# Kernel tuning notes

Hardware: AMD Instinct MI355X
Metric: run time of the kernel (lower is better)

The kernel has to match this reference:

```python
import jax, jax.numpy as jnp
import numpy as np

EMBED_SIZE = 1024
HEADS = 16
HEAD_DIM = EMBED_SIZE // HEADS


def setup_inputs() -> dict:
    key = jax.random.key(0)
    k1, k2, k3, k4 = jax.random.split(key, 4)
    N, L = 4, 2048
    return {
        "values": jax.random.normal(k1, (N, L, EMBED_SIZE), dtype=jnp.float32),
        "keys": jax.random.normal(k2, (N, L, EMBED_SIZE), dtype=jnp.float32),
        "query": jax.random.normal(k3, (N, L, EMBED_SIZE), dtype=jnp.float32),
        "w_out": jax.random.normal(k4, (EMBED_SIZE, EMBED_SIZE), dtype=jnp.float32) * (1.0 / np.sqrt(EMBED_SIZE)),
        "b_out": jnp.zeros((EMBED_SIZE,), dtype=jnp.float32),
    }


def reference(values, keys, query, w_out, b_out):
    N, q_len, _ = query.shape
    v_len = values.shape[1]
    k_len = keys.shape[1]
    # split heads: (N, L, H, D). NOTE: source never applies the per-head
    # q/k/v Linear layers in forward, so raw inputs are used directly.
    v = values.reshape(N, v_len, HEADS, HEAD_DIM)
    k = keys.reshape(N, k_len, HEADS, HEAD_DIM)
    q = query.reshape(N, q_len, HEADS, HEAD_DIM)
    # energy: (N, H, Q, K); scale by sqrt(embed_size) as in the source
    energy = jnp.einsum('nqhd,nkhd->nhqk', q, k)
    attn = jax.nn.softmax(energy / jnp.sqrt(jnp.float32(EMBED_SIZE)), axis=3)
    out = jnp.einsum('nhql,nlhd->nqhd', attn, v).reshape(N, q_len, EMBED_SIZE)
    # fc_out: x @ W.T + b (torch Linear convention)
    return out @ w_out.T + b_out
```

## Files before the change

### kernel.cpp

```cpp
#include <hip/hip_runtime.h>
#include <hip/hip_bf16.h>

#define NB 4
#define LSEQ 2048
#define NH 16
#define HD 64
#define EMB 1024

typedef __attribute__((ext_vector_type(8))) short bf16x8;
typedef __attribute__((ext_vector_type(4))) float f32x4;
typedef __attribute__((ext_vector_type(16))) float f32x16;
typedef __attribute__((ext_vector_type(2))) unsigned int uint2v;

__device__ __forceinline__ unsigned short f2bf(float x) {
    union { float f; unsigned u; } v; v.f = x;
    unsigned r = v.u + 0x7fff + ((v.u >> 16) & 1);
    return (unsigned short)(r >> 16);
}

__device__ __forceinline__ float exp2_fast(float x) {
#if __has_builtin(__builtin_amdgcn_exp2f)
    return __builtin_amdgcn_exp2f(x);
#else
    float r; asm("v_exp_f32 %0, %1\n\ts_nop 1" : "=v"(r) : "v"(x)); return r;
#endif
}

__device__ __forceinline__ unsigned pack_bf2(float lo, float hi) {
    union { __hip_bfloat162 h2; unsigned u; } cv;
    cv.h2 = __float22bfloat162_rn(make_float2(lo, hi));
    return cv.u;
}

__device__ __forceinline__ void plswap(unsigned &a, unsigned &b) {
#if __has_builtin(__builtin_amdgcn_permlane32_swap)
    uint2v r = __builtin_amdgcn_permlane32_swap(a, b, false, false);
    a = r[0]; b = r[1];
#else
    asm volatile("s_nop 0\n\tv_permlane32_swap_b32 %0, %1\n\ts_nop 0"
                 : "+v"(a), "+v"(b));
#endif
}

__device__ __forceinline__ void async16(void* lds, const void* g) {
    __builtin_amdgcn_global_load_lds(
        (const __attribute__((address_space(1))) unsigned int*)g,
        (__attribute__((address_space(3))) unsigned int*)lds, 16, 0, 0);
}

__global__ void wconv_kernel(const float* __restrict__ Wf, unsigned short* __restrict__ Wb) {
    int i = (blockIdx.x * 256 + threadIdx.x) * 4;
    float4 v = *(const float4*)(Wf + i);
    ushort4 o = { f2bf(v.x), f2bf(v.y), f2bf(v.z), f2bf(v.w) };
    *(ushort4*)(Wb + i) = o;
}

__global__ void k_prep(const float* __restrict__ Kf, unsigned short* __restrict__ Kb) {
    int idx = blockIdx.x * 256 + threadIdx.x;
    int c   = idx & 7;
    int key = (idx >> 3) & 2047;
    int h   = (idx >> 14) & 15;
    int n   = idx >> 18;
    const float* src = Kf + (size_t)(n * LSEQ + key) * EMB + h * HD + c * 8;
    float4 a = *(const float4*)src;
    float4 b = *(const float4*)(src + 4);
    unsigned short* dst = Kb + (((size_t)(n * NH + h) * LSEQ + key) << 6)
                             + ((c ^ (key & 7)) << 3);
    ushort4 o0 = { f2bf(a.x), f2bf(a.y), f2bf(a.z), f2bf(a.w) };
    ushort4 o1 = { f2bf(b.x), f2bf(b.y), f2bf(b.z), f2bf(b.w) };
    *(ushort4*)dst = o0;
    *(ushort4*)(dst + 4) = o1;
}

__global__ void v_prep(const float* __restrict__ Vf, unsigned short* __restrict__ Vt) {
    int b = blockIdx.x;
    int kt = b & 31, h = (b >> 5) & 15, n = b >> 9;
    const float* src = Vf + (size_t)(n * LSEQ + kt * 64) * EMB + h * HD;
    unsigned short* dst = Vt + ((size_t)b << 12);
    for (int t = threadIdx.x; t < 512; t += 256) {
        int d = t >> 3, c = t & 7;
        const float* s = src + (size_t)(c * 8) * EMB + d;
        ushort4 o0, o1;
        o0.x = f2bf(s[0 * EMB]); o0.y = f2bf(s[1 * EMB]);
        o0.z = f2bf(s[2 * EMB]); o0.w = f2bf(s[3 * EMB]);
        o1.x = f2bf(s[4 * EMB]); o1.y = f2bf(s[5 * EMB]);
        o1.z = f2bf(s[6 * EMB]); o1.w = f2bf(s[7 * EMB]);
        unsigned short* p = dst + (d << 6) + ((c ^ (d & 7)) << 3);
        *(ushort4*)p = o0;
        *(ushort4*)(p + 4) = o1;
    }
}

__global__ __launch_bounds__(256, 2)
void attn8_kernel(const float* __restrict__ Qq, const unsigned short* __restrict__ Kb,
                  const unsigned short* __restrict__ Vt, unsigned short* __restrict__ X)
{
    __shared__ unsigned short Kl[2][4096];
    __shared__ unsigned short Vl[2][4096];

    const int tid  = threadIdx.x;
    const int lane = tid & 63;
    const int w    = tid >> 6;
    const int l31  = lane & 31;
    const int hl   = lane >> 5;
    const int swz7 = lane & 7;
    const int l    = ((blockIdx.x & 7) << 6) + (blockIdx.x >> 3);
    const int nh   = l >> 3;
    const int qtile = l & 7;
    const int n = nh >> 4, h = nh & 15;
    const int qrow0 = qtile * 256 + w * 64;

    const float qscale = 0.03125f * 1.44269504f;
    bf16x8 qf[2][4];
    #pragma unroll
    for (int g = 0; g < 2; ++g) {
        const float* qp = Qq + (size_t)(n * LSEQ + qrow0 + g * 32 + l31) * EMB + h * HD + hl * 8;
        #pragma unroll
        for (int dk = 0; dk < 4; ++dk) {
            bf16x8 t;
            #pragma unroll
            for (int e = 0; e < 8; ++e) t[e] = (short)f2bf(qp[dk * 16 + e] * qscale);
            qf[g][dk] = t;
        }
    }

    f32x16 oaccT[2][2];
    #pragma unroll
    for (int g = 0; g < 2; ++g)
        #pragma unroll
        for (int db = 0; db < 2; ++db)
            #pragma unroll
            for (int e = 0; e < 16; ++e) oaccT[g][db][e] = 0.f;
    float lp[2] = {0.f, 0.f};

    const unsigned short* kg0 = Kb + ((size_t)nh << 17);
    const unsigned short* vg0 = Vt + ((size_t)nh << 17);
    const int t8 = tid << 3;

    async16(&Kl[0][t8],        kg0 + t8);
    async16(&Kl[0][t8 + 2048], kg0 + t8 + 2048);
    async16(&Vl[0][t8],        vg0 + t8);
    async16(&Vl[0][t8 + 2048], vg0 + t8 + 2048);
    asm volatile("s_waitcnt vmcnt(0)" ::: "memory");
    __syncthreads();

    int cur = 0;
    for (int kt = 0; kt < LSEQ / 64; ++kt) {
        if (kt + 1 < LSEQ / 64) {
            const unsigned short* kg = kg0 + ((kt + 1) << 12) + t8;
            const unsigned short* vg = vg0 + ((kt + 1) << 12) + t8;
            async16(&Kl[cur ^ 1][t8],        kg);
            async16(&Kl[cur ^ 1][t8 + 2048], kg + 2048);
            async16(&Vl[cur ^ 1][t8],        vg);
            async16(&Vl[cur ^ 1][t8 + 2048], vg + 2048);
        }

        #pragma unroll
        for (int kb = 0; kb < 2; ++kb) {
            f32x16 sk[2];
            #pragma unroll
            for (int g = 0; g < 2; ++g)
                #pragma unroll
                for (int e = 0; e < 16; ++e) sk[g][e] = 0.f;
            #pragma unroll
            for (int dk = 0; dk < 4; ++dk) {
                bf16x8 ka = *(const bf16x8*)&Kl[cur][((kb * 32 + l31) << 6) + (((2 * dk + hl) ^ swz7) << 3)];
                #pragma unroll
                for (int g = 0; g < 2; ++g)
                    sk[g] = __builtin_amdgcn_mfma_f32_32x32x16_bf16(ka, qf[g][dk], sk[g], 0, 0, 0);
            }

            unsigned wgt[2][4][2];
            #pragma unroll
            for (int g = 0; g < 2; ++g) {
                float p[16];
                #pragma unroll
                for (int e = 0; e < 16; ++e) p[e] = exp2_fast(sk[g][e]);
                {
                    float t0 = (p[0] + p[1]) + (p[2] + p[3]);
                    float t1 = (p[4] + p[5]) + (p[6] + p[7]);
                    float t2 = (p[8] + p[9]) + (p[10] + p[11]);
                    float t3 = (p[12] + p[13]) + (p[14] + p[15]);
                    lp[g] += (t0 + t1) + (t2 + t3);
                }
                #pragma unroll
                for (int gg = 0; gg < 4; ++gg) {
                    wgt[g][gg][0] = pack_bf2(p[4 * gg + 0], p[4 * gg + 1]);
                    wgt[g][gg][1] = pack_bf2(p[4 * gg + 2], p[4 * gg + 3]);
                }
                plswap(wgt[g][0][0], wgt[g][1][0]); plswap(wgt[g][0][1], wgt[g][1][1]);
                plswap(wgt[g][2][0], wgt[g][3][0]); plswap(wgt[g][2][1], wgt[g][3][1]);
            }

            #pragma unroll
            for (int ks = 0; ks < 2; ++ks) {
                #pragma unroll
                for (int db = 0; db < 2; ++db) {
                    bf16x8 va = *(const bf16x8*)&Vl[cur][((db * 32 + l31) << 6) + (((4 * kb + 2 * ks + hl) ^ swz7) << 3)];
                    #pragma unroll
                    for (int g = 0; g < 2; ++g) {
                        union { unsigned u[4]; bf16x8 v; } pu;
                        pu.u[0] = wgt[g][2 * ks + 0][0];
                        pu.u[1] = wgt[g][2 * ks + 0][1];
                        pu.u[2] = wgt[g][2 * ks + 1][0];
                        pu.u[3] = wgt[g][2 * ks + 1][1];
                        oaccT[g][db] = __builtin_amdgcn_mfma_f32_32x32x16_bf16(va, pu.v, oaccT[g][db], 0, 0, 0);
                    }
                }
            }
        }

        asm volatile("s_waitcnt vmcnt(0)" ::: "memory");
        __syncthreads();
        cur ^= 1;
    }

    #pragma unroll
    for (int g = 0; g < 2; ++g) {
        const float ltot = lp[g] + __shfl_xor(lp[g], 32);
        const float rcp = 1.0f / ltot;
        unsigned ow0[4][2], ow1[4][2];
        #pragma unroll
        for (int gg = 0; gg < 4; ++gg) {
            ow0[gg][0] = pack_bf2(oaccT[g][0][4 * gg + 0] * rcp, oaccT[g][0][4 * gg + 1] * rcp);
            ow0[gg][1] = pack_bf2(oaccT[g][0][4 * gg + 2] * rcp, oaccT[g][0][4 * gg + 3] * rcp);
            ow1[gg][0] = pack_bf2(oaccT[g][1][4 * gg + 0] * rcp, oaccT[g][1][4 * gg + 1] * rcp);
            ow1[gg][1] = pack_bf2(oaccT[g][1][4 * gg + 2] * rcp, oaccT[g][1][4 * gg + 3] * rcp);
        }
        #pragma unroll
        for (int gg = 0; gg < 4; ++gg) {
            plswap(ow0[gg][0], ow1[gg][0]);
            plswap(ow0[gg][1], ow1[gg][1]);
        }
        unsigned short* xrow = X + (size_t)(n * LSEQ + qrow0 + g * 32 + l31) * EMB + h * HD + hl * 32;
        #pragma unroll
        for (int gg = 0; gg < 4; ++gg) {
            uint4 st = { ow0[gg][0], ow0[gg][1], ow1[gg][0], ow1[gg][1] };
            *(uint4*)(xrow + 8 * gg) = st;
        }
    }
}

#define KPAD 72
#define PPAD 72

__global__ __launch_bounds__(256, 2)
void attn_kernel(const float* __restrict__ Vv, const float* __restrict__ Kk,
                 const float* __restrict__ Qq, unsigned short* __restrict__ X)
{
    __shared__ unsigned short Klds[64 * KPAD];
    __shared__ unsigned short Vtlds[64 * KPAD];
    __shared__ unsigned short Plds[4 * 16 * PPAD];

    const int tid  = threadIdx.x;
    const int lane = tid & 63;
    const int w    = tid >> 6;
    const int l15  = lane & 15;
    const int l4   = lane >> 4;
    const int qtile = blockIdx.x;
    const int nh    = blockIdx.y;
    const int n = nh >> 4, h = nh & 15;

    bf16x8 qf[2];
    {
        const int qrow = qtile * 64 + w * 16 + l15;
        const float* qp = Qq + (size_t)(n * LSEQ + qrow) * EMB + h * HD + l4 * 8;
        for (int kk = 0; kk < 2; ++kk) {
            bf16x8 t;
            #pragma unroll
            for (int e = 0; e < 8; ++e) t[e] = (short)f2bf(qp[kk * 32 + e] * 0.03125f);
            qf[kk] = t;
        }
    }

    f32x4 oacc[4];
    #pragma unroll
    for (int f = 0; f < 4; ++f) oacc[f] = (f32x4){0.f, 0.f, 0.f, 0.f};
    float mrun[4], lrun[4];
    #pragma unroll
    for (int r = 0; r < 4; ++r) { mrun[r] = -1e30f; lrun[r] = 0.f; }

    for (int kt = 0; kt < LSEQ / 64; ++kt) {
        __syncthreads();
        for (int i = tid; i < 1024; i += 256) {
            const int row = i >> 4;
            const int c4  = (i & 15) * 4;
            const size_t gb = (size_t)(n * LSEQ + kt * 64 + row) * EMB + h * HD + c4;
            const float4 kv = *(const float4*)(Kk + gb);
            const float4 vv = *(const float4*)(Vv + gb);
            ushort4 k4 = { f2bf(kv.x), f2bf(kv.y), f2bf(kv.z), f2bf(kv.w) };
            *(ushort4*)&Klds[row * KPAD + c4] = k4;
            Vtlds[(c4 + 0) * KPAD + row] = f2bf(vv.x);
            Vtlds[(c4 + 1) * KPAD + row] = f2bf(vv.y);
            Vtlds[(c4 + 2) * KPAD + row] = f2bf(vv.z);
            Vtlds[(c4 + 3) * KPAD + row] = f2bf(vv.w);
        }
        __syncthreads();

        f32x4 s[4];
        #pragma unroll
        for (int f = 0; f < 4; ++f) {
            f32x4 acc = (f32x4){0.f, 0.f, 0.f, 0.f};
            #pragma unroll
            for (int kk = 0; kk < 2; ++kk) {
                bf16x8 kb = *(const bf16x8*)&Klds[(f * 16 + l15) * KPAD + kk * 32 + l4 * 8];
                acc = __builtin_amdgcn_mfma_f32_16x16x32_bf16(qf[kk], kb, acc, 0, 0, 0);
            }
            s[f] = acc;
        }

        float mnew[4], corr[4];
        #pragma unroll
        for (int r = 0; r < 4; ++r) {
            float m0 = fmaxf(fmaxf(s[0][r], s[1][r]), fmaxf(s[2][r], s[3][r]));
            #pragma unroll
            for (int msk = 1; msk < 16; msk <<= 1) m0 = fmaxf(m0, __shfl_xor(m0, msk));
            mnew[r] = fmaxf(mrun[r], m0);
            corr[r] = __expf(mrun[r] - mnew[r]);
        }
        float psum[4] = {0.f, 0.f, 0.f, 0.f};
        #pragma unroll
        for (int f = 0; f < 4; ++f) {
            #pragma unroll
            for (int r = 0; r < 4; ++r) {
                float p = __expf(s[f][r] - mnew[r]);
                psum[r] += p;
                Plds[(w * 16 + l4 * 4 + r) * PPAD + f * 16 + l15] = f2bf(p);
            }
        }
        #pragma unroll
        for (int r = 0; r < 4; ++r) {
            float t = psum[r];
            #pragma unroll
            for (int msk = 1; msk < 16; msk <<= 1) t += __shfl_xor(t, msk);
            lrun[r] = lrun[r] * corr[r] + t;
            mrun[r] = mnew[r];
        }
        #pragma unroll
        for (int f = 0; f < 4; ++f) {
            #pragma unroll
            for (int r = 0; r < 4; ++r) oacc[f][r] *= corr[r];
        }
        __syncthreads();

        #pragma unroll
        for (int ks = 0; ks < 2; ++ks) {
            bf16x8 pa = *(const bf16x8*)&Plds[(w * 16 + l15) * PPAD + ks * 32 + l4 * 8];
            #pragma unroll
            for (int f = 0; f < 4; ++f) {
                bf16x8 vb = *(const bf16x8*)&Vtlds[(f * 16 + l15) * KPAD + ks * 32 + l4 * 8];
                oacc[f] = __builtin_amdgcn_mfma_f32_16x16x32_bf16(pa, vb, oacc[f], 0, 0, 0);
            }
        }
    }

    #pragma unroll
    for (int f = 0; f < 4; ++f) {
        #pragma unroll
        for (int r = 0; r < 4; ++r) {
            const int qrow = qtile * 64 + w * 16 + l4 * 4 + r;
            const float o = oacc[f][r] / lrun[r];
            X[(size_t)(n * LSEQ + qrow) * EMB + h * HD + f * 16 + l15] = f2bf(o);
        }
    }
}

__global__ __launch_bounds__(256, 2)
void proj3_kernel(const unsigned short* __restrict__ X, const unsigned short* __restrict__ Wb,
                  const float* __restrict__ bias, float* __restrict__ out)
{
    __shared__ unsigned short Al[2][8192];
    __shared__ unsigned short Bl[2][8192];

    const int tid  = threadIdx.x;
    const int lane = tid & 63;
    const int w    = tid >> 6;
    const int l15  = lane & 15;
    const int l4   = lane >> 4;
    const int bm = blockIdx.y;
    const int bn = blockIdx.x;
    const int wr = (w >> 1) * 64;
    const int wc = (w & 1) * 64;

    f32x4 acc[4][4];
    #pragma unroll
    for (int i = 0; i < 4; ++i)
        #pragma unroll
        for (int j = 0; j < 4; ++j) acc[i][j] = (f32x4){0.f, 0.f, 0.f, 0.f};

    int srow[4], soff[4];
    #pragma unroll
    for (int j = 0; j < 4; ++j) {
        const int cid = tid + j * 256;
        srow[j] = cid >> 3;
        const int c = cid & 7;
        soff[j] = ((c ^ (srow[j] & 7)) << 3);
    }

#define PROJ_STAGE(buf, k0)                                                          \
    {                                                                                \
        _Pragma("unroll")                                                            \
        for (int j = 0; j < 4; ++j) {                                                \
            const int cid = tid + j * 256;                                           \
            async16(&Al[buf][cid << 3],                                              \
                    &X [(size_t)(bm * 128 + srow[j]) * EMB + (k0) + soff[j]]);       \
            async16(&Bl[buf][cid << 3],                                              \
                    &Wb[(size_t)(bn * 128 + srow[j]) * EMB + (k0) + soff[j]]);       \
        }                                                                            \
    }

    PROJ_STAGE(0, 0)
    asm volatile("s_waitcnt vmcnt(0)" ::: "memory");
    __syncthreads();

    int cur = 0;
    for (int k0 = 0; k0 < EMB; k0 += 64) {
        if (k0 + 64 < EMB) PROJ_STAGE(cur ^ 1, k0 + 64)

        #pragma unroll
        for (int kk = 0; kk < 2; ++kk) {
            bf16x8 af[4], bfr[4];
            #pragma unroll
            for (int i = 0; i < 4; ++i) {
                const int row = wr + i * 16 + l15;
                af[i] = *(const bf16x8*)&Al[cur][(row << 6) + (((kk * 4 + l4) ^ (row & 7)) << 3)];
            }
            #pragma unroll
            for (int j = 0; j < 4; ++j) {
                const int row = wc + j * 16 + l15;
                bfr[j] = *(const bf16x8*)&Bl[cur][(row << 6) + (((kk * 4 + l4) ^ (row & 7)) << 3)];
            }
            #pragma unroll
            for (int i = 0; i < 4; ++i)
                #pragma unroll
                for (int j = 0; j < 4; ++j)
                    acc[i][j] = __builtin_amdgcn_mfma_f32_16x16x32_bf16(af[i], bfr[j], acc[i][j], 0, 0, 0);
        }

        asm volatile("s_waitcnt vmcnt(0)" ::: "memory");
        __syncthreads();
        cur ^= 1;
    }

    #pragma unroll
    for (int i = 0; i < 4; ++i) {
        const int row = bm * 128 + wr + i * 16 + l4 * 4;
        #pragma unroll
        for (int j = 0; j < 4; ++j) {
            const int col = bn * 128 + wc + j * 16 + l15;
            const float bj = bias[col];
            #pragma unroll
            for (int r = 0; r < 4; ++r)
                out[(size_t)(row + r) * EMB + col] = acc[i][j][r] + bj;
        }
    }
}

extern "C" void kernel_launch(void* const* d_in, const int* in_sizes, int n_in,
                              void* d_out, int out_size, void* d_ws, size_t ws_size,
                              hipStream_t stream) {
    const float* Vv   = (const float*)d_in[0];
    const float* Kk   = (const float*)d_in[1];
    const float* Qq   = (const float*)d_in[2];
    const float* Wf   = (const float*)d_in[3];
    const float* bias = (const float*)d_in[4];
    float* out = (float*)d_out;

    unsigned short* X  = (unsigned short*)d_ws;
    unsigned short* Wb = (unsigned short*)((char*)d_ws + (size_t)16 * 1024 * 1024);
    const size_t need = (size_t)50 * 1024 * 1024;

    wconv_kernel<<<dim3(EMB * EMB / 1024), 256, 0, stream>>>(Wf, Wb);

    if (ws_size >= need) {
        unsigned short* Kb = (unsigned short*)((char*)d_ws + (size_t)18 * 1024 * 1024);
        unsigned short* Vt = (unsigned short*)((char*)d_ws + (size_t)34 * 1024 * 1024);
        k_prep<<<dim3(4096), 256, 0, stream>>>(Kk, Kb);
        v_prep<<<dim3(2048), 256, 0, stream>>>(Vv, Vt);
        attn8_kernel<<<dim3(512), 256, 0, stream>>>(Qq, Kb, Vt, X);
    } else {
        attn_kernel<<<dim3(LSEQ / 64, NB * NH), 256, 0, stream>>>(Vv, Kk, Qq, X);
    }

    proj3_kernel<<<dim3(EMB / 128, NB * LSEQ / 128), 256, 0, stream>>>(X, Wb, bias, out);
}
```

Baseline: 138.9 us.

## Transpose V through LDS, double attention K-tile, add setprio and grouped proj tiling

The V preparation kernel now reads coalesced float4 rows into a padded LDS tile and transposes from there, replacing strided global reads. The attention kernel stages 128 keys per iteration instead of 64, which halves the number of barriers and doubles LDS use per block. s_setprio is raised around MFMA sections in both attention and projection. The projection launch is remapped to a 1D grid with a grouped block order meant to improve L2 reuse. The larger LDS footprint may reduce occupancy.

```diff
diff --git a/kernel.cpp b/kernel.cpp
--- a/kernel.cpp
+++ b/kernel.cpp
@@ -72,19 +72,28 @@
     *(ushort4*)(dst + 4) = o1;
 }
 
-__global__ void v_prep(const float* __restrict__ Vf, unsigned short* __restrict__ Vt) {
-    int b = blockIdx.x;
-    int kt = b & 31, h = (b >> 5) & 15, n = b >> 9;
+__global__ void v_prep2(const float* __restrict__ Vf, unsigned short* __restrict__ Vt) {
+    __shared__ float T[64][65];
+    const int tid = threadIdx.x;
+    const int b = blockIdx.x;
+    const int kt = b & 31, h = (b >> 5) & 15, n = b >> 9;
     const float* src = Vf + (size_t)(n * LSEQ + kt * 64) * EMB + h * HD;
     unsigned short* dst = Vt + ((size_t)b << 12);
-    for (int t = threadIdx.x; t < 512; t += 256) {
-        int d = t >> 3, c = t & 7;
-        const float* s = src + (size_t)(c * 8) * EMB + d;
-        ushort4 o0, o1;
-        o0.x = f2bf(s[0 * EMB]); o0.y = f2bf(s[1 * EMB]);
-        o0.z = f2bf(s[2 * EMB]); o0.w = f2bf(s[3 * EMB]);
-        o1.x = f2bf(s[4 * EMB]); o1.y = f2bf(s[5 * EMB]);
-        o1.z = f2bf(s[6 * EMB]); o1.w = f2bf(s[7 * EMB]);
+
+    for (int i = tid; i < 1024; i += 256) {
+        const int key = i >> 4;
+        const int c4  = (i & 15) * 4;
+        const float4 v = *(const float4*)(src + (size_t)key * EMB + c4);
+        T[key][c4 + 0] = v.x; T[key][c4 + 1] = v.y;
+        T[key][c4 + 2] = v.z; T[key][c4 + 3] = v.w;
+    }
+    __syncthreads();
+    for (int i = tid; i < 512; i += 256) {
+        const int d = i >> 3, c = i & 7;
+        ushort4 o0 = { f2bf(T[c * 8 + 0][d]), f2bf(T[c * 8 + 1][d]),
+                       f2bf(T[c * 8 + 2][d]), f2bf(T[c * 8 + 3][d]) };
+        ushort4 o1 = { f2bf(T[c * 8 + 4][d]), f2bf(T[c * 8 + 5][d]),
+                       f2bf(T[c * 8 + 6][d]), f2bf(T[c * 8 + 7][d]) };
         unsigned short* p = dst + (d << 6) + ((c ^ (d & 7)) << 3);
         *(ushort4*)p = o0;
         *(ushort4*)(p + 4) = o1;
@@ -92,11 +101,11 @@
 }
 
 __global__ __launch_bounds__(256, 2)
-void attn8_kernel(const float* __restrict__ Qq, const unsigned short* __restrict__ Kb,
+void attn9_kernel(const float* __restrict__ Qq, const unsigned short* __restrict__ Kb,
                   const unsigned short* __restrict__ Vt, unsigned short* __restrict__ X)
 {
-    __shared__ unsigned short Kl[2][4096];
-    __shared__ unsigned short Vl[2][4096];
+    __shared__ unsigned short Kl[2][8192];
+    __shared__ unsigned short Vl[2][8192];
 
     const int tid  = threadIdx.x;
     const int lane = tid & 63;
@@ -137,31 +146,33 @@
     const unsigned short* vg0 = Vt + ((size_t)nh << 17);
     const int t8 = tid << 3;
 
-    async16(&Kl[0][t8],        kg0 + t8);
-    async16(&Kl[0][t8 + 2048], kg0 + t8 + 2048);
-    async16(&Vl[0][t8],        vg0 + t8);
-    async16(&Vl[0][t8 + 2048], vg0 + t8 + 2048);
+#define ATTN_STAGE(buf, kt)                                                  \
+    {                                                                        \
+        const unsigned short* kg = kg0 + ((kt) << 13) + t8;                  \
+        const unsigned short* vg = vg0 + ((kt) << 13) + t8;                  \
+        _Pragma("unroll")                                                    \
+        for (int j = 0; j < 4; ++j) {                                        \
+            async16(&Kl[buf][t8 + j * 2048], kg + j * 2048);                 \
+            async16(&Vl[buf][t8 + j * 2048], vg + j * 2048);                 \
+        }                                                                    \
+    }
+
+    ATTN_STAGE(0, 0)
     asm volatile("s_waitcnt vmcnt(0)" ::: "memory");
     __syncthreads();
 
     int cur = 0;
-    for (int kt = 0; kt < LSEQ / 64; ++kt) {
-        if (kt + 1 < LSEQ / 64) {
-            const unsigned short* kg = kg0 + ((kt + 1) << 12) + t8;
-            const unsigned short* vg = vg0 + ((kt + 1) << 12) + t8;
-            async16(&Kl[cur ^ 1][t8],        kg);
-            async16(&Kl[cur ^ 1][t8 + 2048], kg + 2048);
-            async16(&Vl[cur ^ 1][t8],        vg);
-            async16(&Vl[cur ^ 1][t8 + 2048], vg + 2048);
-        }
-
-        #pragma unroll
-        for (int kb = 0; kb < 2; ++kb) {
+    for (int kt = 0; kt < LSEQ / 128; ++kt) {
+        if (kt + 1 < LSEQ / 128) ATTN_STAGE(cur ^ 1, kt + 1)
+
+        #pragma unroll
+        for (int kb = 0; kb < 4; ++kb) {
             f32x16 sk[2];
             #pragma unroll
             for (int g = 0; g < 2; ++g)
                 #pragma unroll
                 for (int e = 0; e < 16; ++e) sk[g][e] = 0.f;
+            __builtin_amdgcn_s_setprio(1);
             #pragma unroll
             for (int dk = 0; dk < 4; ++dk) {
                 bf16x8 ka = *(const bf16x8*)&Kl[cur][((kb * 32 + l31) << 6) + (((2 * dk + hl) ^ swz7) << 3)];
@@ -169,6 +180,7 @@
                 for (int g = 0; g < 2; ++g)
                     sk[g] = __builtin_amdgcn_mfma_f32_32x32x16_bf16(ka, qf[g][dk], sk[g], 0, 0, 0);
             }
+            __builtin_amdgcn_s_setprio(0);
 
             unsigned wgt[2][4][2];
             #pragma unroll
@@ -192,11 +204,14 @@
                 plswap(wgt[g][2][0], wgt[g][3][0]); plswap(wgt[g][2][1], wgt[g][3][1]);
             }
 
+            const int vbase = (kb >> 1) << 12;
+            const int kb1   = kb & 1;
+            __builtin_amdgcn_s_setprio(1);
             #pragma unroll
             for (int ks = 0; ks < 2; ++ks) {
                 #pragma unroll
                 for (int db = 0; db < 2; ++db) {
-                    bf16x8 va = *(const bf16x8*)&Vl[cur][((db * 32 + l31) << 6) + (((4 * kb + 2 * ks + hl) ^ swz7) << 3)];
+                    bf16x8 va = *(const bf16x8*)&Vl[cur][vbase + ((db * 32 + l31) << 6) + (((4 * kb1 + 2 * ks + hl) ^ swz7) << 3)];
                     #pragma unroll
                     for (int g = 0; g < 2; ++g) {
                         union { unsigned u[4]; bf16x8 v; } pu;
@@ -208,6 +223,7 @@
                     }
                 }
             }
+            __builtin_amdgcn_s_setprio(0);
         }
 
         asm volatile("s_waitcnt vmcnt(0)" ::: "memory");
@@ -366,7 +382,7 @@
 }
 
 __global__ __launch_bounds__(256, 2)
-void proj3_kernel(const unsigned short* __restrict__ X, const unsigned short* __restrict__ Wb,
+void proj4_kernel(const unsigned short* __restrict__ X, const unsigned short* __restrict__ Wb,
                   const float* __restrict__ bias, float* __restrict__ out)
 {
     __shared__ unsigned short Al[2][8192];
@@ -377,8 +393,9 @@
     const int w    = tid >> 6;
     const int l15  = lane & 15;
     const int l4   = lane >> 4;
-    const int bm = blockIdx.y;
-    const int bn = blockIdx.x;
+    const int bid  = blockIdx.x;
+    const int bm   = (bid & 7) * 8 + ((bid >> 3) & 7);
+    const int bn   = bid >> 6;
     const int wr = (w >> 1) * 64;
     const int wc = (w & 1) * 64;
 
@@ -430,11 +447,13 @@
                 const int row = wc + j * 16 + l15;
                 bfr[j] = *(const bf16x8*)&Bl[cur][(row << 6) + (((kk * 4 + l4) ^ (row & 7)) << 3)];
             }
+            __builtin_amdgcn_s_setprio(1);
             #pragma unroll
             for (int i = 0; i < 4; ++i)
                 #pragma unroll
                 for (int j = 0; j < 4; ++j)
                     acc[i][j] = __builtin_amdgcn_mfma_f32_16x16x32_bf16(af[i], bfr[j], acc[i][j], 0, 0, 0);
+            __builtin_amdgcn_s_setprio(0);
         }
 
         asm volatile("s_waitcnt vmcnt(0)" ::: "memory");
@@ -476,11 +495,11 @@
         unsigned short* Kb = (unsigned short*)((char*)d_ws + (size_t)18 * 1024 * 1024);
         unsigned short* Vt = (unsigned short*)((char*)d_ws + (size_t)34 * 1024 * 1024);
         k_prep<<<dim3(4096), 256, 0, stream>>>(Kk, Kb);
-        v_prep<<<dim3(2048), 256, 0, stream>>>(Vv, Vt);
-        attn8_kernel<<<dim3(512), 256, 0, stream>>>(Qq, Kb, Vt, X);
+        v_prep2<<<dim3(2048), 256, 0, stream>>>(Vv, Vt);
+        attn9_kernel<<<dim3(512), 256, 0, stream>>>(Qq, Kb, Vt, X);
     } else {
         attn_kernel<<<dim3(LSEQ / 64, NB * NH), 256, 0, stream>>>(Vv, Kk, Qq, X);
     }
 
-    proj3_kernel<<<dim3(EMB / 128, NB * LSEQ / 128), 256, 0, stream>>>(X, Wb, bias, out);
-}
+    proj4_kernel<<<dim3(512), 256, 0, stream>>>(X, Wb, bias, out);
+}
```

After: 137.9 us. No clear change (-0.7%).
